# Kernel tuning notes

Measured on AMD Instinct MI355X. Metric: run time of the kernel, lower is better.

Reference implementation:

```python
import jax, jax.numpy as jnp
import numpy as np

N = 100_000      # nodes
E = 1_600_000    # edges
B = 256          # graphs
DIM = 64
EPS = 1e-5


def _batchnorm(h, gamma, beta):
    # BatchNorm1d in training mode: batch mean, biased variance
    mu = jnp.mean(h, axis=0)
    var = jnp.mean((h - mu) ** 2, axis=0)
    return (h - mu) * jax.lax.rsqrt(var + EPS) * gamma + beta


def setup_inputs() -> dict:
    key = jax.random.key(0)
    ks = jax.random.split(key, 12)
    x = jax.random.normal(ks[0], (N, DIM), dtype=jnp.float32)
    edge_index = jax.random.randint(ks[1], (2, E), 0, N, dtype=jnp.int64)
    edge_attr = jax.random.normal(ks[2], (E, DIM), dtype=jnp.float32)
    state = jax.random.normal(ks[3], (B, DIM), dtype=jnp.float32)
    batch = jnp.sort(jax.random.randint(ks[4], (N,), 0, B, dtype=jnp.int64))
    s = 0.05
    params = {
        "W1": jax.random.normal(ks[5], (DIM, 3 * DIM), dtype=jnp.float32) * s,
        "b1": jnp.zeros((DIM,), jnp.float32),
        "g1": jnp.ones((DIM,), jnp.float32),
        "be1": jnp.zeros((DIM,), jnp.float32),
        "W2": jax.random.normal(ks[6], (DIM, DIM), dtype=jnp.float32) * s,
        "b2": jnp.zeros((DIM,), jnp.float32),
        "g2": jnp.ones((DIM,), jnp.float32),
        "be2": jnp.zeros((DIM,), jnp.float32),
        "W3": jax.random.normal(ks[7], (DIM, DIM), dtype=jnp.float32) * s,
        "b3": jnp.zeros((DIM,), jnp.float32),
        "g3": jnp.ones((DIM,), jnp.float32),
        "be3": jnp.zeros((DIM,), jnp.float32),
    }
    return {"x": x, "edge_index": edge_index, "edge_attr": edge_attr,
            "state": state, "batch": batch, **params}


def reference(x, edge_index, edge_attr, state, batch,
              W1, b1, g1, be1, W2, b2, g2, be2, W3, b3, g3, be3):
    n = x.shape[0]
    src = edge_index[0]
    # scatter-mean of edge_attr onto destination-of-src nodes
    sums = jax.ops.segment_sum(edge_attr, src, num_segments=n)
    cnt = jax.ops.segment_sum(jnp.ones((edge_attr.shape[0],), edge_attr.dtype),
                              src, num_segments=n)
    v_mean = sums / jnp.maximum(cnt, 1.0)[:, None]
    comb = jnp.concatenate([x, v_mean, state[batch]], axis=1)  # [N, 3*DIM]
    h = jax.nn.relu(comb @ W1.T + b1)
    h = _batchnorm(h, g1, be1)
    h = jax.nn.relu(h @ W2.T + b2)
    h = _batchnorm(h, g2, be2)
    h = h @ W3.T + b3
    return _batchnorm(h, g3, be3)
```

## Files before the change

kernel.cpp:

```cpp
#include <hip/hip_runtime.h>

#define NN 100000
#define NE 1600000
#define EPSV 1e-5f

typedef float f32x4 __attribute__((ext_vector_type(4)));
typedef short s16x8 __attribute__((ext_vector_type(8)));

__device__ __forceinline__ unsigned short f2bf(float f) {
  unsigned int u = __float_as_uint(f);
  u += 0x7fffu + ((u >> 16) & 1u);
  return (unsigned short)(u >> 16);
}

__device__ __forceinline__ float bf2f(unsigned short s) {
  return __uint_as_float(((unsigned int)s) << 16);
}

__device__ __forceinline__ ushort4 pack4(float4 v) {
  ushort4 s;
  s.x = f2bf(v.x); s.y = f2bf(v.y); s.z = f2bf(v.z); s.w = f2bf(v.w);
  return s;
}

__global__ __launch_bounds__(256) void k_bucket(
    const int* __restrict__ ei, int* __restrict__ cnt, int* __restrict__ eids) {
  int e = blockIdx.x * 256 + threadIdx.x;
  int src = ei[e];
  int pos = atomicAdd(&cnt[src], 1);
  if (pos < 64) eids[(size_t)src * 64 + pos] = e;
}

__global__ __launch_bounds__(256) void k_gather(
    const int* __restrict__ cnt, const int* __restrict__ eids,
    const float4* __restrict__ ea4, ushort4* __restrict__ vmb4) {
  int n = __builtin_amdgcn_readfirstlane(blockIdx.x * 4 + (threadIdx.x >> 6));
  int lane = threadIdx.x & 63;
  int grp = lane >> 4, q = lane & 15;
  const int* elist = eids + (size_t)n * 64;
  int c = cnt[n];
  int m = c < 64 ? c : 64;
  float ax = 0.f, ay = 0.f, az = 0.f, aw = 0.f;
  for (int e = 0; e < m; e += 16) {
    int rm = m - 1;
    int r0 = e + grp, r1 = e + 4 + grp, r2 = e + 8 + grp, r3 = e + 12 + grp;
    int i0 = elist[r0 < m ? r0 : rm];
    int i1 = elist[r1 < m ? r1 : rm];
    int i2 = elist[r2 < m ? r2 : rm];
    int i3 = elist[r3 < m ? r3 : rm];
    float4 v0 = ea4[(size_t)i0 * 16 + q];
    float4 v1 = ea4[(size_t)i1 * 16 + q];
    float4 v2 = ea4[(size_t)i2 * 16 + q];
    float4 v3 = ea4[(size_t)i3 * 16 + q];
    float m0 = r0 < m ? 1.f : 0.f, m1 = r1 < m ? 1.f : 0.f;
    float m2 = r2 < m ? 1.f : 0.f, m3 = r3 < m ? 1.f : 0.f;
    ax += m0 * v0.x + m1 * v1.x + m2 * v2.x + m3 * v3.x;
    ay += m0 * v0.y + m1 * v1.y + m2 * v2.y + m3 * v3.y;
    az += m0 * v0.z + m1 * v1.z + m2 * v2.z + m3 * v3.z;
    aw += m0 * v0.w + m1 * v1.w + m2 * v2.w + m3 * v3.w;
  }
  ax += __shfl_xor(ax, 16); ay += __shfl_xor(ay, 16);
  az += __shfl_xor(az, 16); aw += __shfl_xor(aw, 16);
  ax += __shfl_xor(ax, 32); ay += __shfl_xor(ay, 32);
  az += __shfl_xor(az, 32); aw += __shfl_xor(aw, 32);
  if (lane < 16) {
    float inv = 1.0f / fmaxf((float)c, 1.0f);
    float4 r; r.x = ax * inv; r.y = ay * inv; r.z = az * inv; r.w = aw * inv;
    vmb4[(size_t)n * 16 + lane] = pack4(r);
  }
}

__global__ __launch_bounds__(256) void k_g1(
    const float4* __restrict__ x4, const ushort4* __restrict__ vmb4,
    const float4* __restrict__ state4,
    const int* __restrict__ batch, const float4* __restrict__ w14,
    const float* __restrict__ b1, unsigned short* __restrict__ h1,
    float* __restrict__ Sout, float* __restrict__ Qout) {
  __shared__ unsigned short lc[64][200];
  __shared__ unsigned short lw[64][200];
  __shared__ float ssum[64], ssq[64];
  const int tid = threadIdx.x;
  const int nodeBase = blockIdx.x * 64;
  if (tid < 64) { ssum[tid] = 0.f; ssq[tid] = 0.f; }
#pragma unroll
  for (int i = 0; i < 12; ++i) {
    int idx = tid + i * 256;
    int row = idx / 48, q = idx % 48;
    *(ushort4*)&lw[row][q * 4] = pack4(w14[idx]);
  }
#pragma unroll
  for (int i = 0; i < 4; ++i) {
    int idx = tid + i * 256;
    int node = idx >> 4, q = idx & 15;
    int g = nodeBase + node;
    float4 vx = {0,0,0,0}, vs = {0,0,0,0};
    ushort4 vm = {0,0,0,0};
    if (g < NN) {
      vx = x4[(size_t)g * 16 + q];
      vm = vmb4[(size_t)g * 16 + q];
      int b = batch[g];
      vs = state4[b * 16 + q];
    }
    *(ushort4*)&lc[node][q * 4]       = pack4(vx);
    *(ushort4*)&lc[node][64 + q * 4]  = vm;
    *(ushort4*)&lc[node][128 + q * 4] = pack4(vs);
  }
  __syncthreads();
  const int lane = tid & 63, w = tid >> 6;
  const int rg = lane >> 4, ci = lane & 15;
  f32x4 acc[4] = {{0,0,0,0},{0,0,0,0},{0,0,0,0},{0,0,0,0}};
#pragma unroll
  for (int s = 0; s < 6; ++s) {
    int k0 = 32 * s + rg * 8;
    s16x8 a = *(const s16x8*)&lc[w * 16 + ci][k0];
#pragma unroll
    for (int c = 0; c < 4; ++c) {
      s16x8 b = *(const s16x8*)&lw[c * 16 + ci][k0];
      acc[c] = __builtin_amdgcn_mfma_f32_16x16x32_bf16(a, b, acc[c], 0, 0, 0);
    }
  }
  __syncthreads();
  unsigned short (*lo)[72] = (unsigned short(*)[72])lw;
#pragma unroll
  for (int c = 0; c < 4; ++c) {
    int col = c * 16 + ci;
    float bb = b1[col];
    float ls = 0.f, lq = 0.f;
#pragma unroll
    for (int r = 0; r < 4; ++r) {
      int row = w * 16 + rg * 4 + r;
      float v = fmaxf(acc[c][r] + bb, 0.f);
      lo[row][col] = f2bf(v);
      if (nodeBase + row < NN) { ls += v; lq += v * v; }
    }
    atomicAdd(&ssum[col], ls);
    atomicAdd(&ssq[col], lq);
  }
  __syncthreads();
#pragma unroll
  for (int i = 0; i < 2; ++i) {
    int idx = tid + i * 256;
    int row = idx >> 3, q = idx & 7;
    int g = nodeBase + row;
    if (g < NN) *(s16x8*)&h1[(size_t)g * 64 + q * 8] = *(const s16x8*)&lo[row][q * 8];
  }
  if (tid < 64) {
    unsafeAtomicAdd(&Sout[tid], ssum[tid]);
    unsafeAtomicAdd(&Qout[tid], ssq[tid]);
  }
}

__global__ __launch_bounds__(256) void k_prep(
    const float* __restrict__ Sin, const float* __restrict__ Qin,
    const float* __restrict__ gm, const float* __restrict__ bt,
    const float* __restrict__ W, const float* __restrict__ bias,
    unsigned short* __restrict__ wf, float* __restrict__ dout) {
  __shared__ float lA[64], lC[64], red[256];
  int t = threadIdx.x;
  if (t < 64) {
    float mu = Sin[t] * (1.0f / NN);
    float var = Qin[t] * (1.0f / NN) - mu * mu;
    float a = gm[t] * rsqrtf(var + EPSV);
    lA[t] = a;
    lC[t] = bt[t] - mu * a;
  }
  __syncthreads();
#pragma unroll
  for (int i = 0; i < 16; ++i) {
    int idx = t + i * 256;
    wf[idx] = f2bf(W[idx] * lA[idx & 63]);
  }
  int j = t >> 2, p = t & 3;
  const float* Wr = W + j * 64 + p * 16;
  float s = 0.f;
#pragma unroll
  for (int k = 0; k < 16; ++k) s += lC[p * 16 + k] * Wr[k];
  red[t] = s;
  __syncthreads();
  if (t < 64) dout[t] = bias[t] + red[t * 4] + red[t * 4 + 1] + red[t * 4 + 2] + red[t * 4 + 3];
}

template <bool RELU>
__global__ __launch_bounds__(256) void k_gemm64(
    const s16x8* __restrict__ A8,
    const s16x8* __restrict__ w8,
    const float* __restrict__ d,
    unsigned short* __restrict__ Obf,
    float* __restrict__ Sout, float* __restrict__ Qout) {
  __shared__ unsigned short la[64][72];
  __shared__ unsigned short lwf[64][72];
  __shared__ float ssum[64], ssq[64];
  const int tid = threadIdx.x;
  const int nodeBase = blockIdx.x * 64;
  if (tid < 64) { ssum[tid] = 0.f; ssq[tid] = 0.f; }
#pragma unroll
  for (int i = 0; i < 2; ++i) {
    int idx = tid + i * 256;
    int row = idx >> 3, q = idx & 7;
    int g = nodeBase + row;
    s16x8 v = {};
    if (g < NN) v = A8[(size_t)g * 8 + q];
    *(s16x8*)&la[row][q * 8] = v;
  }
#pragma unroll
  for (int i = 0; i < 2; ++i) {
    int idx = tid + i * 256;
    int j = idx >> 3, q = idx & 7;
    *(s16x8*)&lwf[j][q * 8] = w8[idx];
  }
  __syncthreads();
  const int lane = tid & 63, w = tid >> 6;
  const int rg = lane >> 4, ci = lane & 15;
  f32x4 acc[4] = {{0,0,0,0},{0,0,0,0},{0,0,0,0},{0,0,0,0}};
#pragma unroll
  for (int s = 0; s < 2; ++s) {
    int k0 = 32 * s + rg * 8;
    s16x8 a = *(const s16x8*)&la[w * 16 + ci][k0];
#pragma unroll
    for (int c = 0; c < 4; ++c) {
      s16x8 b = *(const s16x8*)&lwf[c * 16 + ci][k0];
      acc[c] = __builtin_amdgcn_mfma_f32_16x16x32_bf16(a, b, acc[c], 0, 0, 0);
    }
  }
  __syncthreads();
  unsigned short (*lo)[72] = (unsigned short(*)[72])la;
#pragma unroll
  for (int c = 0; c < 4; ++c) {
    int col = c * 16 + ci;
    float dd = d[col];
    float ls = 0.f, lq = 0.f;
#pragma unroll
    for (int r = 0; r < 4; ++r) {
      int row = w * 16 + rg * 4 + r;
      float v = acc[c][r] + dd;
      if (RELU) v = fmaxf(v, 0.f);
      lo[row][col] = f2bf(v);
      if (nodeBase + row < NN) { ls += v; lq += v * v; }
    }
    atomicAdd(&ssum[col], ls);
    atomicAdd(&ssq[col], lq);
  }
  __syncthreads();
#pragma unroll
  for (int i = 0; i < 2; ++i) {
    int idx = tid + i * 256;
    int row = idx >> 3, q = idx & 7;
    int g = nodeBase + row;
    if (g < NN) *(s16x8*)&Obf[(size_t)g * 64 + q * 8] = *(const s16x8*)&lo[row][q * 8];
  }
  if (tid < 64) {
    unsafeAtomicAdd(&Sout[tid], ssum[tid]);
    unsafeAtomicAdd(&Qout[tid], ssq[tid]);
  }
}

__global__ __launch_bounds__(256) void k_bn3(
    const s16x8* __restrict__ h3b, const float* __restrict__ gm,
    const float* __restrict__ bt, const float* __restrict__ S,
    const float* __restrict__ Q, float4* __restrict__ out) {
  __shared__ float lA[64], lC[64];
  const int tid = threadIdx.x;
  if (tid < 64) {
    float mu = S[tid] * (1.0f / NN);
    float var = Q[tid] * (1.0f / NN) - mu * mu;
    float a = gm[tid] * rsqrtf(var + EPSV);
    lA[tid] = a;
    lC[tid] = bt[tid] - mu * a;
  }
  __syncthreads();
  const int total = NN * 8;
  for (int idx = blockIdx.x * 256 + tid; idx < total; idx += gridDim.x * 256) {
    s16x8 v = h3b[idx];
    int k = (idx & 7) * 8;
    float4 o0, o1;
    o0.x = bf2f((unsigned short)v[0]) * lA[k]     + lC[k];
    o0.y = bf2f((unsigned short)v[1]) * lA[k + 1] + lC[k + 1];
    o0.z = bf2f((unsigned short)v[2]) * lA[k + 2] + lC[k + 2];
    o0.w = bf2f((unsigned short)v[3]) * lA[k + 3] + lC[k + 3];
    o1.x = bf2f((unsigned short)v[4]) * lA[k + 4] + lC[k + 4];
    o1.y = bf2f((unsigned short)v[5]) * lA[k + 5] + lC[k + 5];
    o1.z = bf2f((unsigned short)v[6]) * lA[k + 6] + lC[k + 6];
    o1.w = bf2f((unsigned short)v[7]) * lA[k + 7] + lC[k + 7];
    out[idx * 2]     = o0;
    out[idx * 2 + 1] = o1;
  }
}

extern "C" void kernel_launch(void* const* d_in, const int* in_sizes, int n_in,
                              void* d_out, int out_size, void* d_ws, size_t ws_size,
                              hipStream_t stream) {
  const float* x     = (const float*)d_in[0];
  const int*   ei    = (const int*)d_in[1];
  const float* state = (const float*)d_in[3];
  const int*   batch = (const int*)d_in[4];
  const float* W1  = (const float*)d_in[5];
  const float* b1  = (const float*)d_in[6];
  const float* g1  = (const float*)d_in[7];
  const float* be1 = (const float*)d_in[8];
  const float* W2  = (const float*)d_in[9];
  const float* b2  = (const float*)d_in[10];
  const float* g2  = (const float*)d_in[11];
  const float* be2 = (const float*)d_in[12];
  const float* W3  = (const float*)d_in[13];
  const float* b3  = (const float*)d_in[14];
  const float* g3  = (const float*)d_in[15];
  const float* be3 = (const float*)d_in[16];
  const float* ea  = (const float*)d_in[2];

  char* ws = (char*)d_ws;
  int*   cnt  = (int*)ws;
  float* S1   = (float*)(ws + 400000);
  float* Q1 = S1 + 64;
  float* S2 = S1 + 128;
  float* Q2 = S1 + 192;
  float* S3 = S1 + 256;
  float* Q3 = S1 + 320;
  unsigned short* w2f = (unsigned short*)(ws + 401536);
  float*          d2  = (float*)(ws + 409728);
  unsigned short* w3f = (unsigned short*)(ws + 409984);
  float*          d3  = (float*)(ws + 418176);
  int*            eids = (int*)(ws + 418432);
  unsigned short* h3b  = (unsigned short*)(ws + 418432);
  unsigned short* vmb  = (unsigned short*)(ws + 26018432);
  unsigned short* h2   = (unsigned short*)(ws + 26018432);
  unsigned short* h1   = (unsigned short*)(ws + 38818432);

  hipMemsetAsync(ws, 0, 401536, stream);

  k_bucket<<<NE / 256, 256, 0, stream>>>(ei, cnt, eids);
  k_gather<<<NN / 4, 256, 0, stream>>>(cnt, eids, (const float4*)ea, (ushort4*)vmb);

  const int nblk = (NN + 63) / 64;
  k_g1<<<nblk, 256, 0, stream>>>((const float4*)x, (const ushort4*)vmb,
                                 (const float4*)state, batch, (const float4*)W1,
                                 b1, h1, S1, Q1);
  k_prep<<<1, 256, 0, stream>>>(S1, Q1, g1, be1, W2, b2, w2f, d2);
  k_gemm64<true><<<nblk, 256, 0, stream>>>(
      (const s16x8*)h1, (const s16x8*)w2f, d2, h2, S2, Q2);
  k_prep<<<1, 256, 0, stream>>>(S2, Q2, g2, be2, W3, b3, w3f, d3);
  k_gemm64<false><<<nblk, 256, 0, stream>>>(
      (const s16x8*)h2, (const s16x8*)w3f, d3, h3b, S3, Q3);
  k_bn3<<<2048, 256, 0, stream>>>((const s16x8*)h3b, g3, be3, S3, Q3, (float4*)d_out);
}
```

Before: 385.7 us.

## Fuse MLP and batchnorm stages into one cooperative persistent kernel with LDS-resident activations

Replaces the separate layer-1 GEMM, two prep kernels, two 64x64 GEMMs and the final batchnorm kernel with a single cooperative kernel of 256 blocks. Each block keeps its up to 7 tiles of 64-node activations in shared memory across all layers and uses grid.sync for the batchnorm statistics. This removes the global round trips of h1, h2 and h3 and several launches. In exchange, occupancy is limited to one 256-thread block per CU and three grid-wide barriers are added. The gather kernel is also changed to a fixed 2048-block grid where each wave processes 13 nodes.

```diff
diff --git a/kernel.cpp b/kernel.cpp
--- a/kernel.cpp
+++ b/kernel.cpp
@@ -1,8 +1,14 @@
 #include <hip/hip_runtime.h>
+#include <hip/hip_cooperative_groups.h>
+
+namespace cg = cooperative_groups;
 
 #define NN 100000
 #define NE 1600000
 #define EPSV 1e-5f
+#define NBLK 256
+#define NTILES 1563
+#define MAXT 7
 
 typedef float f32x4 __attribute__((ext_vector_type(4)));
 typedef short s16x8 __attribute__((ext_vector_type(8)));
@@ -34,255 +40,304 @@
 __global__ __launch_bounds__(256) void k_gather(
     const int* __restrict__ cnt, const int* __restrict__ eids,
     const float4* __restrict__ ea4, ushort4* __restrict__ vmb4) {
-  int n = __builtin_amdgcn_readfirstlane(blockIdx.x * 4 + (threadIdx.x >> 6));
+  int wid = (blockIdx.x * 256 + threadIdx.x) >> 6;
   int lane = threadIdx.x & 63;
   int grp = lane >> 4, q = lane & 15;
-  const int* elist = eids + (size_t)n * 64;
-  int c = cnt[n];
-  int m = c < 64 ? c : 64;
-  float ax = 0.f, ay = 0.f, az = 0.f, aw = 0.f;
-  for (int e = 0; e < m; e += 16) {
-    int rm = m - 1;
-    int r0 = e + grp, r1 = e + 4 + grp, r2 = e + 8 + grp, r3 = e + 12 + grp;
-    int i0 = elist[r0 < m ? r0 : rm];
-    int i1 = elist[r1 < m ? r1 : rm];
-    int i2 = elist[r2 < m ? r2 : rm];
-    int i3 = elist[r3 < m ? r3 : rm];
-    float4 v0 = ea4[(size_t)i0 * 16 + q];
-    float4 v1 = ea4[(size_t)i1 * 16 + q];
-    float4 v2 = ea4[(size_t)i2 * 16 + q];
-    float4 v3 = ea4[(size_t)i3 * 16 + q];
-    float m0 = r0 < m ? 1.f : 0.f, m1 = r1 < m ? 1.f : 0.f;
-    float m2 = r2 < m ? 1.f : 0.f, m3 = r3 < m ? 1.f : 0.f;
-    ax += m0 * v0.x + m1 * v1.x + m2 * v2.x + m3 * v3.x;
-    ay += m0 * v0.y + m1 * v1.y + m2 * v2.y + m3 * v3.y;
-    az += m0 * v0.z + m1 * v1.z + m2 * v2.z + m3 * v3.z;
-    aw += m0 * v0.w + m1 * v1.w + m2 * v2.w + m3 * v3.w;
-  }
-  ax += __shfl_xor(ax, 16); ay += __shfl_xor(ay, 16);
-  az += __shfl_xor(az, 16); aw += __shfl_xor(aw, 16);
-  ax += __shfl_xor(ax, 32); ay += __shfl_xor(ay, 32);
-  az += __shfl_xor(az, 32); aw += __shfl_xor(aw, 32);
-  if (lane < 16) {
-    float inv = 1.0f / fmaxf((float)c, 1.0f);
-    float4 r; r.x = ax * inv; r.y = ay * inv; r.z = az * inv; r.w = aw * inv;
-    vmb4[(size_t)n * 16 + lane] = pack4(r);
-  }
-}
-
-__global__ __launch_bounds__(256) void k_g1(
-    const float4* __restrict__ x4, const ushort4* __restrict__ vmb4,
-    const float4* __restrict__ state4,
-    const int* __restrict__ batch, const float4* __restrict__ w14,
-    const float* __restrict__ b1, unsigned short* __restrict__ h1,
-    float* __restrict__ Sout, float* __restrict__ Qout) {
+  int n0 = wid * 13;
+  int nend = n0 + 13 < NN ? n0 + 13 : NN;
+  for (int n = n0; n < nend; ++n) {
+    const int* elist = eids + (size_t)n * 64;
+    int c = cnt[n];
+    int m = c < 64 ? c : 64;
+    float ax = 0.f, ay = 0.f, az = 0.f, aw = 0.f;
+    for (int e = 0; e < m; e += 16) {
+      int rm = m - 1;
+      int r0 = e + grp, r1 = e + 4 + grp, r2 = e + 8 + grp, r3 = e + 12 + grp;
+      int i0 = elist[r0 < m ? r0 : rm];
+      int i1 = elist[r1 < m ? r1 : rm];
+      int i2 = elist[r2 < m ? r2 : rm];
+      int i3 = elist[r3 < m ? r3 : rm];
+      float4 v0 = ea4[(size_t)i0 * 16 + q];
+      float4 v1 = ea4[(size_t)i1 * 16 + q];
+      float4 v2 = ea4[(size_t)i2 * 16 + q];
+      float4 v3 = ea4[(size_t)i3 * 16 + q];
+      float m0 = r0 < m ? 1.f : 0.f, m1 = r1 < m ? 1.f : 0.f;
+      float m2 = r2 < m ? 1.f : 0.f, m3 = r3 < m ? 1.f : 0.f;
+      ax += m0 * v0.x + m1 * v1.x + m2 * v2.x + m3 * v3.x;
+      ay += m0 * v0.y + m1 * v1.y + m2 * v2.y + m3 * v3.y;
+      az += m0 * v0.z + m1 * v1.z + m2 * v2.z + m3 * v3.z;
+      aw += m0 * v0.w + m1 * v1.w + m2 * v2.w + m3 * v3.w;
+    }
+    ax += __shfl_xor(ax, 16); ay += __shfl_xor(ay, 16);
+    az += __shfl_xor(az, 16); aw += __shfl_xor(aw, 16);
+    ax += __shfl_xor(ax, 32); ay += __shfl_xor(ay, 32);
+    az += __shfl_xor(az, 32); aw += __shfl_xor(aw, 32);
+    if (lane < 16) {
+      float inv = 1.0f / fmaxf((float)c, 1.0f);
+      float4 r; r.x = ax * inv; r.y = ay * inv; r.z = az * inv; r.w = aw * inv;
+      vmb4[(size_t)n * 16 + lane] = pack4(r);
+    }
+  }
+}
+
+struct MegaArgs {
+  const float4* x4; const ushort4* vmb4; const float4* state4; const int* batch;
+  const float4* w14; const float* b1;
+  const float* W2; const float* b2; const float* g1; const float* be1;
+  const float* W3; const float* b3; const float* g2; const float* be2;
+  const float* g3; const float* be3;
+  float* S1; float* Q1; float* S2; float* Q2; float* S3; float* Q3;
+  float4* out4;
+};
+
+__global__ __launch_bounds__(256, 1) void k_mega(MegaArgs A) {
+  __shared__ unsigned short ht[MAXT][64][72];
   __shared__ unsigned short lc[64][200];
   __shared__ unsigned short lw[64][200];
   __shared__ float ssum[64], ssq[64];
+  __shared__ float lA[64], lC[64], ld[64], red[256];
+  cg::grid_group grid = cg::this_grid();
   const int tid = threadIdx.x;
-  const int nodeBase = blockIdx.x * 64;
-  if (tid < 64) { ssum[tid] = 0.f; ssq[tid] = 0.f; }
+  const int b = blockIdx.x;
+  const int ntiles = (NTILES - b + NBLK - 1) / NBLK;
+  const int lane = tid & 63, w = tid >> 6;
+  const int rg = lane >> 4, ci = lane & 15;
+  unsigned short (*lw2)[72] = (unsigned short(*)[72])lw;
+
 #pragma unroll
   for (int i = 0; i < 12; ++i) {
     int idx = tid + i * 256;
     int row = idx / 48, q = idx % 48;
-    *(ushort4*)&lw[row][q * 4] = pack4(w14[idx]);
-  }
-#pragma unroll
-  for (int i = 0; i < 4; ++i) {
-    int idx = tid + i * 256;
-    int node = idx >> 4, q = idx & 15;
-    int g = nodeBase + node;
-    float4 vx = {0,0,0,0}, vs = {0,0,0,0};
-    ushort4 vm = {0,0,0,0};
-    if (g < NN) {
-      vx = x4[(size_t)g * 16 + q];
-      vm = vmb4[(size_t)g * 16 + q];
-      int b = batch[g];
-      vs = state4[b * 16 + q];
-    }
-    *(ushort4*)&lc[node][q * 4]       = pack4(vx);
-    *(ushort4*)&lc[node][64 + q * 4]  = vm;
-    *(ushort4*)&lc[node][128 + q * 4] = pack4(vs);
-  }
-  __syncthreads();
-  const int lane = tid & 63, w = tid >> 6;
-  const int rg = lane >> 4, ci = lane & 15;
-  f32x4 acc[4] = {{0,0,0,0},{0,0,0,0},{0,0,0,0},{0,0,0,0}};
-#pragma unroll
-  for (int s = 0; s < 6; ++s) {
-    int k0 = 32 * s + rg * 8;
-    s16x8 a = *(const s16x8*)&lc[w * 16 + ci][k0];
+    *(ushort4*)&lw[row][q * 4] = pack4(A.w14[idx]);
+  }
+  if (tid < 64) { ssum[tid] = 0.f; ssq[tid] = 0.f; }
+
+  {
+    float ls[4] = {0,0,0,0}, lq[4] = {0,0,0,0};
+    for (int i = 0; i < ntiles; ++i) {
+      int nodeBase = (b + i * NBLK) * 64;
+#pragma unroll
+      for (int it = 0; it < 4; ++it) {
+        int idx = tid + it * 256;
+        int node = idx >> 4, q = idx & 15;
+        int g = nodeBase + node;
+        float4 vx = {0,0,0,0}, vs = {0,0,0,0};
+        ushort4 vm = {0,0,0,0};
+        if (g < NN) {
+          vx = A.x4[(size_t)g * 16 + q];
+          vm = A.vmb4[(size_t)g * 16 + q];
+          vs = A.state4[A.batch[g] * 16 + q];
+        }
+        *(ushort4*)&lc[node][q * 4]       = pack4(vx);
+        *(ushort4*)&lc[node][64 + q * 4]  = vm;
+        *(ushort4*)&lc[node][128 + q * 4] = pack4(vs);
+      }
+      __syncthreads();
+      f32x4 acc[4] = {{0,0,0,0},{0,0,0,0},{0,0,0,0},{0,0,0,0}};
+#pragma unroll
+      for (int s = 0; s < 6; ++s) {
+        int k0 = 32 * s + rg * 8;
+        s16x8 a = *(const s16x8*)&lc[w * 16 + ci][k0];
+#pragma unroll
+        for (int c = 0; c < 4; ++c) {
+          s16x8 bb = *(const s16x8*)&lw[c * 16 + ci][k0];
+          acc[c] = __builtin_amdgcn_mfma_f32_16x16x32_bf16(a, bb, acc[c], 0, 0, 0);
+        }
+      }
+#pragma unroll
+      for (int c = 0; c < 4; ++c) {
+        int col = c * 16 + ci;
+        float bb = A.b1[col];
+#pragma unroll
+        for (int r = 0; r < 4; ++r) {
+          int row = w * 16 + rg * 4 + r;
+          float v = fmaxf(acc[c][r] + bb, 0.f);
+          ht[i][row][col] = f2bf(v);
+          if (nodeBase + row < NN) { ls[c] += v; lq[c] += v * v; }
+        }
+      }
+      __syncthreads();
+    }
 #pragma unroll
     for (int c = 0; c < 4; ++c) {
-      s16x8 b = *(const s16x8*)&lw[c * 16 + ci][k0];
-      acc[c] = __builtin_amdgcn_mfma_f32_16x16x32_bf16(a, b, acc[c], 0, 0, 0);
-    }
-  }
-  __syncthreads();
-  unsigned short (*lo)[72] = (unsigned short(*)[72])lw;
-#pragma unroll
-  for (int c = 0; c < 4; ++c) {
-    int col = c * 16 + ci;
-    float bb = b1[col];
-    float ls = 0.f, lq = 0.f;
-#pragma unroll
-    for (int r = 0; r < 4; ++r) {
-      int row = w * 16 + rg * 4 + r;
-      float v = fmaxf(acc[c][r] + bb, 0.f);
-      lo[row][col] = f2bf(v);
-      if (nodeBase + row < NN) { ls += v; lq += v * v; }
-    }
-    atomicAdd(&ssum[col], ls);
-    atomicAdd(&ssq[col], lq);
-  }
-  __syncthreads();
-#pragma unroll
-  for (int i = 0; i < 2; ++i) {
-    int idx = tid + i * 256;
-    int row = idx >> 3, q = idx & 7;
-    int g = nodeBase + row;
-    if (g < NN) *(s16x8*)&h1[(size_t)g * 64 + q * 8] = *(const s16x8*)&lo[row][q * 8];
-  }
-  if (tid < 64) {
-    unsafeAtomicAdd(&Sout[tid], ssum[tid]);
-    unsafeAtomicAdd(&Qout[tid], ssq[tid]);
-  }
-}
-
-__global__ __launch_bounds__(256) void k_prep(
-    const float* __restrict__ Sin, const float* __restrict__ Qin,
-    const float* __restrict__ gm, const float* __restrict__ bt,
-    const float* __restrict__ W, const float* __restrict__ bias,
-    unsigned short* __restrict__ wf, float* __restrict__ dout) {
-  __shared__ float lA[64], lC[64], red[256];
-  int t = threadIdx.x;
-  if (t < 64) {
-    float mu = Sin[t] * (1.0f / NN);
-    float var = Qin[t] * (1.0f / NN) - mu * mu;
-    float a = gm[t] * rsqrtf(var + EPSV);
-    lA[t] = a;
-    lC[t] = bt[t] - mu * a;
-  }
-  __syncthreads();
-#pragma unroll
-  for (int i = 0; i < 16; ++i) {
-    int idx = t + i * 256;
-    wf[idx] = f2bf(W[idx] * lA[idx & 63]);
-  }
-  int j = t >> 2, p = t & 3;
-  const float* Wr = W + j * 64 + p * 16;
-  float s = 0.f;
-#pragma unroll
-  for (int k = 0; k < 16; ++k) s += lC[p * 16 + k] * Wr[k];
-  red[t] = s;
-  __syncthreads();
-  if (t < 64) dout[t] = bias[t] + red[t * 4] + red[t * 4 + 1] + red[t * 4 + 2] + red[t * 4 + 3];
-}
-
-template <bool RELU>
-__global__ __launch_bounds__(256) void k_gemm64(
-    const s16x8* __restrict__ A8,
-    const s16x8* __restrict__ w8,
-    const float* __restrict__ d,
-    unsigned short* __restrict__ Obf,
-    float* __restrict__ Sout, float* __restrict__ Qout) {
-  __shared__ unsigned short la[64][72];
-  __shared__ unsigned short lwf[64][72];
-  __shared__ float ssum[64], ssq[64];
-  const int tid = threadIdx.x;
-  const int nodeBase = blockIdx.x * 64;
-  if (tid < 64) { ssum[tid] = 0.f; ssq[tid] = 0.f; }
-#pragma unroll
-  for (int i = 0; i < 2; ++i) {
-    int idx = tid + i * 256;
-    int row = idx >> 3, q = idx & 7;
-    int g = nodeBase + row;
-    s16x8 v = {};
-    if (g < NN) v = A8[(size_t)g * 8 + q];
-    *(s16x8*)&la[row][q * 8] = v;
-  }
-#pragma unroll
-  for (int i = 0; i < 2; ++i) {
-    int idx = tid + i * 256;
-    int j = idx >> 3, q = idx & 7;
-    *(s16x8*)&lwf[j][q * 8] = w8[idx];
-  }
-  __syncthreads();
-  const int lane = tid & 63, w = tid >> 6;
-  const int rg = lane >> 4, ci = lane & 15;
-  f32x4 acc[4] = {{0,0,0,0},{0,0,0,0},{0,0,0,0},{0,0,0,0}};
-#pragma unroll
-  for (int s = 0; s < 2; ++s) {
-    int k0 = 32 * s + rg * 8;
-    s16x8 a = *(const s16x8*)&la[w * 16 + ci][k0];
+      atomicAdd(&ssum[c * 16 + ci], ls[c]);
+      atomicAdd(&ssq[c * 16 + ci], lq[c]);
+    }
+    __syncthreads();
+    if (tid < 64) {
+      unsafeAtomicAdd(&A.S1[tid], ssum[tid]);
+      unsafeAtomicAdd(&A.Q1[tid], ssq[tid]);
+    }
+    __threadfence();
+  }
+  grid.sync();
+
+  {
+    if (tid < 64) {
+      float Sv = atomicAdd(&A.S1[tid], 0.0f);
+      float Qv = atomicAdd(&A.Q1[tid], 0.0f);
+      float mu = Sv * (1.0f / NN);
+      float var = Qv * (1.0f / NN) - mu * mu;
+      float a = A.g1[tid] * rsqrtf(var + EPSV);
+      lA[tid] = a; lC[tid] = A.be1[tid] - mu * a;
+      ssum[tid] = 0.f; ssq[tid] = 0.f;
+    }
+    __syncthreads();
+#pragma unroll
+    for (int i = 0; i < 16; ++i) {
+      int idx = tid + i * 256;
+      lw2[idx >> 6][idx & 63] = f2bf(A.W2[idx] * lA[idx & 63]);
+    }
+    {
+      int j = tid >> 2, p = tid & 3;
+      const float* Wr = A.W2 + j * 64 + p * 16;
+      float s = 0.f;
+#pragma unroll
+      for (int k = 0; k < 16; ++k) s += lC[p * 16 + k] * Wr[k];
+      red[tid] = s;
+    }
+    __syncthreads();
+    if (tid < 64) ld[tid] = A.b2[tid] + red[tid*4] + red[tid*4+1] + red[tid*4+2] + red[tid*4+3];
+    __syncthreads();
+
+    float ls[4] = {0,0,0,0}, lq[4] = {0,0,0,0};
+    for (int i = 0; i < ntiles; ++i) {
+      int nodeBase = (b + i * NBLK) * 64;
+      f32x4 acc[4] = {{0,0,0,0},{0,0,0,0},{0,0,0,0},{0,0,0,0}};
+#pragma unroll
+      for (int s = 0; s < 2; ++s) {
+        int k0 = 32 * s + rg * 8;
+        s16x8 a = *(const s16x8*)&ht[i][w * 16 + ci][k0];
+#pragma unroll
+        for (int c = 0; c < 4; ++c) {
+          s16x8 bb = *(const s16x8*)&lw2[c * 16 + ci][k0];
+          acc[c] = __builtin_amdgcn_mfma_f32_16x16x32_bf16(a, bb, acc[c], 0, 0, 0);
+        }
+      }
+#pragma unroll
+      for (int c = 0; c < 4; ++c) {
+        int col = c * 16 + ci;
+        float dd = ld[col];
+#pragma unroll
+        for (int r = 0; r < 4; ++r) {
+          int row = w * 16 + rg * 4 + r;
+          float v = fmaxf(acc[c][r] + dd, 0.f);
+          ht[i][row][col] = f2bf(v);
+          if (nodeBase + row < NN) { ls[c] += v; lq[c] += v * v; }
+        }
+      }
+    }
 #pragma unroll
     for (int c = 0; c < 4; ++c) {
-      s16x8 b = *(const s16x8*)&lwf[c * 16 + ci][k0];
-      acc[c] = __builtin_amdgcn_mfma_f32_16x16x32_bf16(a, b, acc[c], 0, 0, 0);
-    }
-  }
-  __syncthreads();
-  unsigned short (*lo)[72] = (unsigned short(*)[72])la;
-#pragma unroll
-  for (int c = 0; c < 4; ++c) {
-    int col = c * 16 + ci;
-    float dd = d[col];
-    float ls = 0.f, lq = 0.f;
-#pragma unroll
-    for (int r = 0; r < 4; ++r) {
-      int row = w * 16 + rg * 4 + r;
-      float v = acc[c][r] + dd;
-      if (RELU) v = fmaxf(v, 0.f);
-      lo[row][col] = f2bf(v);
-      if (nodeBase + row < NN) { ls += v; lq += v * v; }
-    }
-    atomicAdd(&ssum[col], ls);
-    atomicAdd(&ssq[col], lq);
-  }
-  __syncthreads();
-#pragma unroll
-  for (int i = 0; i < 2; ++i) {
-    int idx = tid + i * 256;
-    int row = idx >> 3, q = idx & 7;
-    int g = nodeBase + row;
-    if (g < NN) *(s16x8*)&Obf[(size_t)g * 64 + q * 8] = *(const s16x8*)&lo[row][q * 8];
-  }
-  if (tid < 64) {
-    unsafeAtomicAdd(&Sout[tid], ssum[tid]);
-    unsafeAtomicAdd(&Qout[tid], ssq[tid]);
-  }
-}
-
-__global__ __launch_bounds__(256) void k_bn3(
-    const s16x8* __restrict__ h3b, const float* __restrict__ gm,
-    const float* __restrict__ bt, const float* __restrict__ S,
-    const float* __restrict__ Q, float4* __restrict__ out) {
-  __shared__ float lA[64], lC[64];
-  const int tid = threadIdx.x;
-  if (tid < 64) {
-    float mu = S[tid] * (1.0f / NN);
-    float var = Q[tid] * (1.0f / NN) - mu * mu;
-    float a = gm[tid] * rsqrtf(var + EPSV);
-    lA[tid] = a;
-    lC[tid] = bt[tid] - mu * a;
-  }
-  __syncthreads();
-  const int total = NN * 8;
-  for (int idx = blockIdx.x * 256 + tid; idx < total; idx += gridDim.x * 256) {
-    s16x8 v = h3b[idx];
-    int k = (idx & 7) * 8;
-    float4 o0, o1;
-    o0.x = bf2f((unsigned short)v[0]) * lA[k]     + lC[k];
-    o0.y = bf2f((unsigned short)v[1]) * lA[k + 1] + lC[k + 1];
-    o0.z = bf2f((unsigned short)v[2]) * lA[k + 2] + lC[k + 2];
-    o0.w = bf2f((unsigned short)v[3]) * lA[k + 3] + lC[k + 3];
-    o1.x = bf2f((unsigned short)v[4]) * lA[k + 4] + lC[k + 4];
-    o1.y = bf2f((unsigned short)v[5]) * lA[k + 5] + lC[k + 5];
-    o1.z = bf2f((unsigned short)v[6]) * lA[k + 6] + lC[k + 6];
-    o1.w = bf2f((unsigned short)v[7]) * lA[k + 7] + lC[k + 7];
-    out[idx * 2]     = o0;
-    out[idx * 2 + 1] = o1;
+      atomicAdd(&ssum[c * 16 + ci], ls[c]);
+      atomicAdd(&ssq[c * 16 + ci], lq[c]);
+    }
+    __syncthreads();
+    if (tid < 64) {
+      unsafeAtomicAdd(&A.S2[tid], ssum[tid]);
+      unsafeAtomicAdd(&A.Q2[tid], ssq[tid]);
+    }
+    __threadfence();
+  }
+  grid.sync();
+
+  {
+    if (tid < 64) {
+      float Sv = atomicAdd(&A.S2[tid], 0.0f);
+      float Qv = atomicAdd(&A.Q2[tid], 0.0f);
+      float mu = Sv * (1.0f / NN);
+      float var = Qv * (1.0f / NN) - mu * mu;
+      float a = A.g2[tid] * rsqrtf(var + EPSV);
+      lA[tid] = a; lC[tid] = A.be2[tid] - mu * a;
+      ssum[tid] = 0.f; ssq[tid] = 0.f;
+    }
+    __syncthreads();
+#pragma unroll
+    for (int i = 0; i < 16; ++i) {
+      int idx = tid + i * 256;
+      lw2[idx >> 6][idx & 63] = f2bf(A.W3[idx] * lA[idx & 63]);
+    }
+    {
+      int j = tid >> 2, p = tid & 3;
+      const float* Wr = A.W3 + j * 64 + p * 16;
+      float s = 0.f;
+#pragma unroll
+      for (int k = 0; k < 16; ++k) s += lC[p * 16 + k] * Wr[k];
+      red[tid] = s;
+    }
+    __syncthreads();
+    if (tid < 64) ld[tid] = A.b3[tid] + red[tid*4] + red[tid*4+1] + red[tid*4+2] + red[tid*4+3];
+    __syncthreads();
+
+    float ls[4] = {0,0,0,0}, lq[4] = {0,0,0,0};
+    for (int i = 0; i < ntiles; ++i) {
+      int nodeBase = (b + i * NBLK) * 64;
+      f32x4 acc[4] = {{0,0,0,0},{0,0,0,0},{0,0,0,0},{0,0,0,0}};
+#pragma unroll
+      for (int s = 0; s < 2; ++s) {
+        int k0 = 32 * s + rg * 8;
+        s16x8 a = *(const s16x8*)&ht[i][w * 16 + ci][k0];
+#pragma unroll
+        for (int c = 0; c < 4; ++c) {
+          s16x8 bb = *(const s16x8*)&lw2[c * 16 + ci][k0];
+          acc[c] = __builtin_amdgcn_mfma_f32_16x16x32_bf16(a, bb, acc[c], 0, 0, 0);
+        }
+      }
+#pragma unroll
+      for (int c = 0; c < 4; ++c) {
+        int col = c * 16 + ci;
+        float dd = ld[col];
+#pragma unroll
+        for (int r = 0; r < 4; ++r) {
+          int row = w * 16 + rg * 4 + r;
+          float v = acc[c][r] + dd;
+          ht[i][row][col] = f2bf(v);
+          if (nodeBase + row < NN) { ls[c] += v; lq[c] += v * v; }
+        }
+      }
+    }
+#pragma unroll
+    for (int c = 0; c < 4; ++c) {
+      atomicAdd(&ssum[c * 16 + ci], ls[c]);
+      atomicAdd(&ssq[c * 16 + ci], lq[c]);
+    }
+    __syncthreads();
+    if (tid < 64) {
+      unsafeAtomicAdd(&A.S3[tid], ssum[tid]);
+      unsafeAtomicAdd(&A.Q3[tid], ssq[tid]);
+    }
+    __threadfence();
+  }
+  grid.sync();
+
+  {
+    if (tid < 64) {
+      float Sv = atomicAdd(&A.S3[tid], 0.0f);
+      float Qv = atomicAdd(&A.Q3[tid], 0.0f);
+      float mu = Sv * (1.0f / NN);
+      float var = Qv * (1.0f / NN) - mu * mu;
+      float a = A.g3[tid] * rsqrtf(var + EPSV);
+      lA[tid] = a; lC[tid] = A.be3[tid] - mu * a;
+    }
+    __syncthreads();
+    for (int i = 0; i < ntiles; ++i) {
+      int nodeBase = (b + i * NBLK) * 64;
+#pragma unroll
+      for (int it = 0; it < 4; ++it) {
+        int idx = tid + it * 256;
+        int row = idx >> 4, q = idx & 15;
+        int g = nodeBase + row;
+        if (g < NN) {
+          int k = q * 4;
+          float4 o;
+          o.x = bf2f(ht[i][row][k])     * lA[k]     + lC[k];
+          o.y = bf2f(ht[i][row][k + 1]) * lA[k + 1] + lC[k + 1];
+          o.z = bf2f(ht[i][row][k + 2]) * lA[k + 2] + lC[k + 2];
+          o.w = bf2f(ht[i][row][k + 3]) * lA[k + 3] + lC[k + 3];
+          A.out4[(size_t)g * 16 + q] = o;
+        }
+      }
+    }
   }
 }
 
@@ -291,21 +346,9 @@
                               hipStream_t stream) {
   const float* x     = (const float*)d_in[0];
   const int*   ei    = (const int*)d_in[1];
+  const float* ea    = (const float*)d_in[2];
   const float* state = (const float*)d_in[3];
   const int*   batch = (const int*)d_in[4];
-  const float* W1  = (const float*)d_in[5];
-  const float* b1  = (const float*)d_in[6];
-  const float* g1  = (const float*)d_in[7];
-  const float* be1 = (const float*)d_in[8];
-  const float* W2  = (const float*)d_in[9];
-  const float* b2  = (const float*)d_in[10];
-  const float* g2  = (const float*)d_in[11];
-  const float* be2 = (const float*)d_in[12];
-  const float* W3  = (const float*)d_in[13];
-  const float* b3  = (const float*)d_in[14];
-  const float* g3  = (const float*)d_in[15];
-  const float* be3 = (const float*)d_in[16];
-  const float* ea  = (const float*)d_in[2];
 
   char* ws = (char*)d_ws;
   int*   cnt  = (int*)ws;
@@ -315,30 +358,25 @@
   float* Q2 = S1 + 192;
   float* S3 = S1 + 256;
   float* Q3 = S1 + 320;
-  unsigned short* w2f = (unsigned short*)(ws + 401536);
-  float*          d2  = (float*)(ws + 409728);
-  unsigned short* w3f = (unsigned short*)(ws + 409984);
-  float*          d3  = (float*)(ws + 418176);
-  int*            eids = (int*)(ws + 418432);
-  unsigned short* h3b  = (unsigned short*)(ws + 418432);
+  int*            eids = (int*)(ws + 401536);
   unsigned short* vmb  = (unsigned short*)(ws + 26018432);
-  unsigned short* h2   = (unsigned short*)(ws + 26018432);
-  unsigned short* h1   = (unsigned short*)(ws + 38818432);
 
   hipMemsetAsync(ws, 0, 401536, stream);
 
   k_bucket<<<NE / 256, 256, 0, stream>>>(ei, cnt, eids);
-  k_gather<<<NN / 4, 256, 0, stream>>>(cnt, eids, (const float4*)ea, (ushort4*)vmb);
-
-  const int nblk = (NN + 63) / 64;
-  k_g1<<<nblk, 256, 0, stream>>>((const float4*)x, (const ushort4*)vmb,
-                                 (const float4*)state, batch, (const float4*)W1,
-                                 b1, h1, S1, Q1);
-  k_prep<<<1, 256, 0, stream>>>(S1, Q1, g1, be1, W2, b2, w2f, d2);
-  k_gemm64<true><<<nblk, 256, 0, stream>>>(
-      (const s16x8*)h1, (const s16x8*)w2f, d2, h2, S2, Q2);
-  k_prep<<<1, 256, 0, stream>>>(S2, Q2, g2, be2, W3, b3, w3f, d3);
-  k_gemm64<false><<<nblk, 256, 0, stream>>>(
-      (const s16x8*)h2, (const s16x8*)w3f, d3, h3b, S3, Q3);
-  k_bn3<<<2048, 256, 0, stream>>>((const s16x8*)h3b, g3, be3, S3, Q3, (float4*)d_out);
-}
+  k_gather<<<2048, 256, 0, stream>>>(cnt, eids, (const float4*)ea, (ushort4*)vmb);
+
+  MegaArgs ma;
+  ma.x4 = (const float4*)x; ma.vmb4 = (const ushort4*)vmb;
+  ma.state4 = (const float4*)state; ma.batch = batch;
+  ma.w14 = (const float4*)d_in[5]; ma.b1 = (const float*)d_in[6];
+  ma.W2 = (const float*)d_in[9]; ma.b2 = (const float*)d_in[10];
+  ma.g1 = (const float*)d_in[7]; ma.be1 = (const float*)d_in[8];
+  ma.W3 = (const float*)d_in[13]; ma.b3 = (const float*)d_in[14];
+  ma.g2 = (const float*)d_in[11]; ma.be2 = (const float*)d_in[12];
+  ma.g3 = (const float*)d_in[15]; ma.be3 = (const float*)d_in[16];
+  ma.S1 = S1; ma.Q1 = Q1; ma.S2 = S2; ma.Q2 = Q2; ma.S3 = S3; ma.Q3 = Q3;
+  ma.out4 = (float4*)d_out;
+  void* kargs[] = {&ma};
+  hipLaunchCooperativeKernel((const void*)k_mega, dim3(NBLK), dim3(256), kargs, 0u, stream);
+}
```

Measured after the change: 448.6 us. 1.16x slower.
